# Kernel optimization log

Measured on AMD Instinct MI355X. Metric: run time of the kernel, lower is better.

## Reference

```python
import jax, jax.numpy as jnp
import numpy as np

N = 50000
E = 1_600_000


def spmm(edge_index, edge_weight, support, num_nodes):
    # adj[i, j] = w for (i=row, j=col); out[i] = sum_j adj[i,j] * support[j]
    row, col = edge_index[0], edge_index[1]
    msgs = support[col] * edge_weight[:, None]  # [E, d] gather + scale
    return jax.ops.segment_sum(msgs, row, num_segments=num_nodes)


def setup_inputs() -> dict:
    key = jax.random.key(0)
    ks = jax.random.split(key, 7)
    x = jax.random.normal(ks[0], (N, 128), dtype=jnp.float32)
    edge_index = jax.random.randint(ks[1], (2, E), 0, N, dtype=jnp.int64)
    edge_weight = jax.random.uniform(ks[2], (E,), dtype=jnp.float32)
    W1 = jax.random.normal(ks[3], (128, 128), dtype=jnp.float32) * (1.0 / np.sqrt(128))
    b1 = jax.random.normal(ks[4], (128,), dtype=jnp.float32) * (1.0 / np.sqrt(128))
    W2 = jax.random.normal(ks[5], (128, 40), dtype=jnp.float32) * (1.0 / np.sqrt(40))
    b2 = jax.random.normal(ks[6], (40,), dtype=jnp.float32) * (1.0 / np.sqrt(40))
    return {"x": x, "edge_index": edge_index, "edge_weight": edge_weight,
            "W1": W1, "b1": b1, "W2": W2, "b2": b2}


def reference(x, edge_index, edge_weight, W1, b1, W2, b2):
    n = x.shape[0]
    # layer 1: GraphConvolution + ReLU (dropout p=0.0 -> no-op)
    h = spmm(edge_index, edge_weight, x @ W1, n) + b1
    h = jax.nn.relu(h)
    # layer 2: GraphConvolution
    out = spmm(edge_index, edge_weight, h @ W2, n) + b2
    return jax.nn.log_softmax(out, axis=1)
```

## Files before the change

kernel.cpp:

```cpp
#include <hip/hip_runtime.h>
#include <hip/hip_fp16.h>
#include <math.h>

#define N_NODES 50000
#define N_EDGES 1600000
#define D1 128
#define D2 40
#define D2P 64
#define BROWS 128
#define NB 391
#define CHUNK 6250

typedef __attribute__((ext_vector_type(8))) short bf16x8;
typedef __attribute__((ext_vector_type(4))) float f32x4;

__device__ __forceinline__ void bf16_split(float v, unsigned short& h, unsigned short& l) {
    unsigned u = __float_as_uint(v);
    unsigned r = u + 0x7fffu + ((u >> 16) & 1u);
    h = (unsigned short)(r >> 16);
    float hf = __uint_as_float((unsigned)h << 16);
    float lof = v - hf;
    unsigned u2 = __float_as_uint(lof);
    unsigned r2 = u2 + 0x7fffu + ((u2 >> 16) & 1u);
    l = (unsigned short)(r2 >> 16);
}

__device__ __forceinline__ int detect_is64_block(const unsigned int* ei) {
    __shared__ int any;
    if (threadIdx.x == 0) any = 0;
    __syncthreads();
    int a = 0;
    for (int i = threadIdx.x; i < 2048; i += 256) a |= (ei[2 * i + 1] != 0u);
    if (a) any = 1;
    __syncthreads();
    return any ? 0 : 1;
}

__device__ __forceinline__ int edge_row(const unsigned int* ei, int e, int is64) {
    return (int)(is64 ? ei[2 * e] : ei[e]);
}
__device__ __forceinline__ int edge_col(const unsigned int* ei, int e, int is64) {
    return (int)(is64 ? ei[2 * (N_EDGES + e)] : ei[N_EDGES + e]);
}

__global__ __launch_bounds__(256) void prep_k(const unsigned int* __restrict__ ei,
                                              unsigned int* __restrict__ gbhp,
                                              const float* __restrict__ W1,
                                              unsigned short* __restrict__ wh1,
                                              unsigned short* __restrict__ wl1,
                                              const float* __restrict__ W2,
                                              unsigned short* __restrict__ wh2,
                                              unsigned short* __restrict__ wl2) {
    int b = blockIdx.x, t = threadIdx.x;
    if (b < 64) {
        int idx = b * 256 + t;
        int k = idx >> 7, n = idx & 127;
        unsigned short h, l;
        bf16_split(W1[k * 128 + n], h, l);
        int nt = n >> 4, ks = k >> 5;
        int lane = (n & 15) | (((k >> 3) & 3) << 4);
        int j = k & 7;
        int dst = ((nt * 4 + ks) * 64 + lane) * 8 + j;
        wh1[dst] = h;
        wl1[dst] = l;
    } else if (b < 96) {
        int idx = (b - 64) * 256 + t;
        int k = idx >> 6, n = idx & 63;
        float v = (n < D2) ? W2[k * D2 + n] : 0.f;
        unsigned short h, l;
        bf16_split(v, h, l);
        int nt = n >> 4, ks = k >> 5;
        int lane = (n & 15) | (((k >> 3) & 3) << 4);
        int j = k & 7;
        int dst = ((nt * 4 + ks) * 64 + lane) * 8 + j;
        wh2[dst] = h;
        wl2[dst] = l;
    } else {
        int is64 = detect_is64_block(ei);
        __shared__ unsigned int bh[NB];
        for (int i = t; i < NB; i += 256) bh[i] = 0;
        __syncthreads();
        int e0 = (b - 96) * CHUNK, e1 = e0 + CHUNK;
        for (int e = e0 + t; e < e1; e += 256) {
            atomicAdd(&bh[edge_row(ei, e, is64) >> 7], 1u);
        }
        __syncthreads();
        for (int i = t; i < NB; i += 256) {
            if (bh[i]) atomicAdd(&gbhp[i * 16], bh[i]);
        }
    }
}

__global__ __launch_bounds__(512) void bscan_k(const unsigned int* __restrict__ gbhp,
                                               int* __restrict__ bbase,
                                               unsigned int* __restrict__ bcurp) {
    __shared__ unsigned int s[512];
    int t = threadIdx.x;
    unsigned int v = (t < NB) ? gbhp[t * 16] : 0u;
    s[t] = v;
    __syncthreads();
    for (int off = 1; off < 512; off <<= 1) {
        unsigned int add = (t >= off) ? s[t - off] : 0u;
        __syncthreads();
        s[t] += add;
        __syncthreads();
    }
    if (t < NB) {
        unsigned int excl = s[t] - v;
        bbase[t] = (int)excl;
        bcurp[t * 16] = excl;
    }
    if (t == NB - 1) bbase[NB] = (int)s[t];
}

__global__ __launch_bounds__(256) void work1_k(const unsigned int* __restrict__ ei,
                                               const float* __restrict__ ew,
                                               unsigned int* __restrict__ bcurp,
                                               uint2* __restrict__ tmp8,
                                               const float* __restrict__ x,
                                               const unsigned short* __restrict__ wh,
                                               const unsigned short* __restrict__ wl,
                                               __half* __restrict__ Ah) {
    int b = blockIdx.x, t = threadIdx.x;
    if (b < 256) {
        int is64 = detect_is64_block(ei);
        __shared__ unsigned int lh[NB];
        __shared__ unsigned int lcur[NB];
        for (int i = t; i < NB; i += 256) lh[i] = 0;
        __syncthreads();
        int e0 = b * CHUNK, e1 = e0 + CHUNK;
        for (int e = e0 + t; e < e1; e += 256) {
            atomicAdd(&lh[edge_row(ei, e, is64) >> 7], 1u);
        }
        __syncthreads();
        for (int i = t; i < NB; i += 256) {
            if (lh[i]) lcur[i] = atomicAdd(&bcurp[i * 16], lh[i]);
        }
        __syncthreads();
        for (int e = e0 + t; e < e1; e += 256) {
            int r = edge_row(ei, e, is64);
            int c = edge_col(ei, e, is64);
            int bk = r >> 7;
            unsigned int p = atomicAdd(&lcur[bk], 1u);
            uint2 rec;
            rec.x = ((unsigned int)(r & 127) << 24) | (unsigned int)c;
            rec.y = __float_as_uint(ew[e]);
            tmp8[p] = rec;
        }
    } else {
        int gb = b - 256;
        int w = t >> 6, l = t & 63;
        int row0 = gb * 64 + w * 16;
        int arow = row0 + (l & 15);
        if (arow > N_NODES - 1) arow = N_NODES - 1;
        int kbase = (l >> 4) * 8;
        bf16x8 ah[4], al[4];
#pragma unroll
        for (int ks = 0; ks < 4; ++ks) {
            const float* px = &x[arow * D1 + ks * 32 + kbase];
            float4 v0 = *reinterpret_cast<const float4*>(px);
            float4 v1 = *reinterpret_cast<const float4*>(px + 4);
            float vv[8] = {v0.x, v0.y, v0.z, v0.w, v1.x, v1.y, v1.z, v1.w};
#pragma unroll
            for (int j = 0; j < 8; ++j) {
                unsigned short h, lo2;
                bf16_split(vv[j], h, lo2);
                ah[ks][j] = (short)h;
                al[ks][j] = (short)lo2;
            }
        }
        f32x4 acc[8];
#pragma unroll
        for (int nt = 0; nt < 8; ++nt) acc[nt] = (f32x4)(0.f);
#pragma unroll
        for (int nt = 0; nt < 8; ++nt) {
#pragma unroll
            for (int ks = 0; ks < 4; ++ks) {
                int fo = ((nt * 4 + ks) * 64 + l) * 8;
                bf16x8 bh = *reinterpret_cast<const bf16x8*>(&wh[fo]);
                bf16x8 bl = *reinterpret_cast<const bf16x8*>(&wl[fo]);
                acc[nt] = __builtin_amdgcn_mfma_f32_16x16x32_bf16(ah[ks], bh, acc[nt], 0, 0, 0);
                acc[nt] = __builtin_amdgcn_mfma_f32_16x16x32_bf16(ah[ks], bl, acc[nt], 0, 0, 0);
                acc[nt] = __builtin_amdgcn_mfma_f32_16x16x32_bf16(al[ks], bh, acc[nt], 0, 0, 0);
            }
        }
        int crow0 = row0 + (l >> 4) * 4;
        int ccol = l & 15;
#pragma unroll
        for (int nt = 0; nt < 8; ++nt) {
#pragma unroll
            for (int r = 0; r < 4; ++r) {
                int rr = crow0 + r;
                if (rr < N_NODES) Ah[rr * D1 + nt * 16 + ccol] = __float2half_rn(acc[nt][r]);
            }
        }
    }
}

__global__ __launch_bounds__(256) void csr_k(const uint2* __restrict__ tmp8,
                                             const int* __restrict__ bbase,
                                             int* __restrict__ rowptr,
                                             uint2* __restrict__ colwS) {
    __shared__ unsigned int rcnt[BROWS];
    __shared__ unsigned int loff[BROWS];
    __shared__ unsigned int lcur[BROWS];
    int b = blockIdx.x;
    int t = threadIdx.x;
    int lo = bbase[b], hi = bbase[b + 1];
    int r0 = b * BROWS;
    int nrows = N_NODES - r0;
    if (nrows > BROWS) nrows = BROWS;
    if (t < BROWS) rcnt[t] = 0;
    __syncthreads();
    for (int j = lo + t; j < hi; j += 256) {
        atomicAdd(&rcnt[tmp8[j].x >> 24], 1u);
    }
    __syncthreads();
    if (t < BROWS) loff[t] = rcnt[t];
    __syncthreads();
    for (int off = 1; off < BROWS; off <<= 1) {
        unsigned int add = (t >= off && t < BROWS) ? loff[t - off] : 0u;
        __syncthreads();
        if (t < BROWS) loff[t] += add;
        __syncthreads();
    }
    if (t < BROWS) {
        unsigned int excl = loff[t] - rcnt[t];
        if (t < nrows) rowptr[r0 + t] = lo + (int)excl;
        lcur[t] = (unsigned int)lo + excl;
    }
    if (b == NB - 1 && t == 0) rowptr[N_NODES] = hi;
    __syncthreads();
    for (int j = lo + t; j < hi; j += 256) {
        uint2 rec = tmp8[j];
        unsigned int rl = rec.x >> 24;
        unsigned int p = atomicAdd(&lcur[rl], 1u);
        uint2 cw;
        cw.x = rec.x & 0xFFFFu;
        cw.y = rec.y;
        colwS[p] = cw;
    }
}

__global__ __launch_bounds__(256) void spmm1_k(const __half* __restrict__ Ah,
                                               const int* __restrict__ rowptr,
                                               const uint2* __restrict__ colwS,
                                               float* __restrict__ B) {
    int t = threadIdx.x;
    int r = blockIdx.x * 4 + (t >> 6);
    int lane = t & 63;
    int half = lane >> 5;
    int cg = lane & 31;
    int s = rowptr[r], e = rowptr[r + 1];
    float4 acc = {0.f, 0.f, 0.f, 0.f};
#pragma unroll 4
    for (int j = s + half; j < e; j += 2) {
        uint2 cw = colwS[j];
        float w = __uint_as_float(cw.y);
        uint2 q = *reinterpret_cast<const uint2*>(&Ah[cw.x * D1 + cg * 4]);
        float2 f0 = __half22float2(*reinterpret_cast<const __half2*>(&q.x));
        float2 f1 = __half22float2(*reinterpret_cast<const __half2*>(&q.y));
        acc.x += w * f0.x;
        acc.y += w * f0.y;
        acc.z += w * f1.x;
        acc.w += w * f1.y;
    }
    acc.x += __shfl_xor(acc.x, 32);
    acc.y += __shfl_xor(acc.y, 32);
    acc.z += __shfl_xor(acc.z, 32);
    acc.w += __shfl_xor(acc.w, 32);
    if (half == 0) *reinterpret_cast<float4*>(&B[r * D1 + cg * 4]) = acc;
}

__global__ __launch_bounds__(256) void gemm2_k(const float* __restrict__ Bm,
                                               const float* __restrict__ b1,
                                               const unsigned short* __restrict__ wh,
                                               const unsigned short* __restrict__ wl,
                                               __half* __restrict__ Gh) {
    int t = threadIdx.x;
    int w = t >> 6, l = t & 63;
    int row0 = blockIdx.x * 64 + w * 16;
    int arow = row0 + (l & 15);
    if (arow > N_NODES - 1) arow = N_NODES - 1;
    int kbase = (l >> 4) * 8;
    bf16x8 ah[4], al[4];
#pragma unroll
    for (int ks = 0; ks < 4; ++ks) {
        const float* pb = &Bm[arow * D1 + ks * 32 + kbase];
        const float* pb1 = &b1[ks * 32 + kbase];
        float4 v0 = *reinterpret_cast<const float4*>(pb);
        float4 v1 = *reinterpret_cast<const float4*>(pb + 4);
        float4 c0 = *reinterpret_cast<const float4*>(pb1);
        float4 c1 = *reinterpret_cast<const float4*>(pb1 + 4);
        float vv[8] = {v0.x + c0.x, v0.y + c0.y, v0.z + c0.z, v0.w + c0.w,
                       v1.x + c1.x, v1.y + c1.y, v1.z + c1.z, v1.w + c1.w};
#pragma unroll
        for (int j = 0; j < 8; ++j) {
            float rv = vv[j] > 0.f ? vv[j] : 0.f;
            unsigned short h, lo2;
            bf16_split(rv, h, lo2);
            ah[ks][j] = (short)h;
            al[ks][j] = (short)lo2;
        }
    }
    f32x4 acc[4];
#pragma unroll
    for (int nt = 0; nt < 4; ++nt) acc[nt] = (f32x4)(0.f);
#pragma unroll
    for (int nt = 0; nt < 4; ++nt) {
#pragma unroll
        for (int ks = 0; ks < 4; ++ks) {
            int fo = ((nt * 4 + ks) * 64 + l) * 8;
            bf16x8 bh = *reinterpret_cast<const bf16x8*>(&wh[fo]);
            bf16x8 bl = *reinterpret_cast<const bf16x8*>(&wl[fo]);
            acc[nt] = __builtin_amdgcn_mfma_f32_16x16x32_bf16(ah[ks], bh, acc[nt], 0, 0, 0);
            acc[nt] = __builtin_amdgcn_mfma_f32_16x16x32_bf16(ah[ks], bl, acc[nt], 0, 0, 0);
            acc[nt] = __builtin_amdgcn_mfma_f32_16x16x32_bf16(al[ks], bh, acc[nt], 0, 0, 0);
        }
    }
    int crow0 = row0 + (l >> 4) * 4;
    int ccol = l & 15;
#pragma unroll
    for (int nt = 0; nt < 4; ++nt) {
        int col = nt * 16 + ccol;
#pragma unroll
        for (int r = 0; r < 4; ++r) {
            int rr = crow0 + r;
            if (rr < N_NODES) Gh[rr * D2P + col] = __float2half_rn(acc[nt][r]);
        }
    }
}

__global__ __launch_bounds__(256) void spmm2lsm_k(const __half* __restrict__ Gh,
                                                  const int* __restrict__ rowptr,
                                                  const uint2* __restrict__ colwS,
                                                  const float* __restrict__ b2,
                                                  float* __restrict__ out) {
    int t = threadIdx.x;
    int r = blockIdx.x * 4 + (t >> 6);
    int lane = t & 63;
    int slot = lane >> 4;
    int li = lane & 15;
    int s = rowptr[r], e = rowptr[r + 1];
    float4 acc = {0.f, 0.f, 0.f, 0.f};
#pragma unroll 2
    for (int j0 = s; j0 < e; j0 += 4) {
        uint2 cwv = colwS[min(j0 + (lane & 3), e - 1)];
        int j = j0 + slot;
        if (j < e) {
            unsigned cx = __shfl(cwv.x, slot);
            float wv = __uint_as_float(__shfl(cwv.y, slot));
            uint2 q = reinterpret_cast<const uint2*>(&Gh[cx * D2P])[li];
            float2 f0 = __half22float2(*reinterpret_cast<const __half2*>(&q.x));
            float2 f1 = __half22float2(*reinterpret_cast<const __half2*>(&q.y));
            acc.x += wv * f0.x;
            acc.y += wv * f0.y;
            acc.z += wv * f1.x;
            acc.w += wv * f1.y;
        }
    }
    acc.x += __shfl_down(acc.x, 32);
    acc.y += __shfl_down(acc.y, 32);
    acc.z += __shfl_down(acc.z, 32);
    acc.w += __shfl_down(acc.w, 32);
    acc.x += __shfl_down(acc.x, 16);
    acc.y += __shfl_down(acc.y, 16);
    acc.z += __shfl_down(acc.z, 16);
    acc.w += __shfl_down(acc.w, 16);
    bool valid = (lane < 16) && (li < 10);
    float4 v4 = {-INFINITY, -INFINITY, -INFINITY, -INFINITY};
    if (valid) {
        float4 bv = *reinterpret_cast<const float4*>(&b2[li * 4]);
        v4.x = acc.x + bv.x;
        v4.y = acc.y + bv.y;
        v4.z = acc.z + bv.z;
        v4.w = acc.w + bv.w;
    }
    float m = fmaxf(fmaxf(v4.x, v4.y), fmaxf(v4.z, v4.w));
#pragma unroll
    for (int off = 1; off < 16; off <<= 1) m = fmaxf(m, __shfl_xor(m, off));
    float ex = valid ? expf(v4.x - m) + expf(v4.y - m) + expf(v4.z - m) + expf(v4.w - m) : 0.f;
#pragma unroll
    for (int off = 1; off < 16; off <<= 1) ex += __shfl_xor(ex, off);
    float lse = m + logf(ex);
    if (valid) {
        float4 o;
        o.x = v4.x - lse;
        o.y = v4.y - lse;
        o.z = v4.z - lse;
        o.w = v4.w - lse;
        *reinterpret_cast<float4*>(&out[r * D2 + li * 4]) = o;
    }
}

extern "C" void kernel_launch(void* const* d_in, const int* in_sizes, int n_in,
                              void* d_out, int out_size, void* d_ws, size_t ws_size,
                              hipStream_t stream) {
    const float* x = (const float*)d_in[0];
    const unsigned int* ei = (const unsigned int*)d_in[1];
    const float* ew = (const float*)d_in[2];
    const float* W1 = (const float*)d_in[3];
    const float* b1 = (const float*)d_in[4];
    const float* W2 = (const float*)d_in[5];
    const float* b2 = (const float*)d_in[6];
    float* out = (float*)d_out;

    char* w = (char*)d_ws;
    __half* Ah = (__half*)w;
    float* B = (float*)(w + 12800000);
    uint2* tmp8 = (uint2*)(w + 12800000);
    __half* Gh = (__half*)(w + 38400000);
    uint2* colwS = (uint2*)(w + 44800000);
    int* rowptr = (int*)(w + 57600000);
    int* bbase = (int*)(w + 57800064);
    unsigned int* bcurp = (unsigned int*)(w + 57801664);
    unsigned int* gbhp = (unsigned int*)(w + 57826688);
    unsigned short* wh1 = (unsigned short*)(w + 57851712);
    unsigned short* wl1 = (unsigned short*)(w + 57884480);
    unsigned short* wh2 = (unsigned short*)(w + 57917248);
    unsigned short* wl2 = (unsigned short*)(w + 57933632);

    hipMemsetAsync(gbhp, 0, NB * 64, stream);
    prep_k<<<352, 256, 0, stream>>>(ei, gbhp, W1, wh1, wl1, W2, wh2, wl2);
    bscan_k<<<1, 512, 0, stream>>>(gbhp, bbase, bcurp);
    work1_k<<<1038, 256, 0, stream>>>(ei, ew, bcurp, tmp8, x, wh1, wl1, Ah);
    csr_k<<<NB, 256, 0, stream>>>(tmp8, bbase, rowptr, colwS);

    spmm1_k<<<N_NODES / 4, 256, 0, stream>>>(Ah, rowptr, colwS, B);
    gemm2_k<<<782, 256, 0, stream>>>(B, b1, wh2, wl2, Gh);
    spmm2lsm_k<<<N_NODES / 4, 256, 0, stream>>>(Gh, rowptr, colwS, b2, out);
}
```

Baseline: 276.4 us.

## Bin edges per chunk in LDS, store hidden layer as fp16, remap spmm2 lanes

CSR construction is restructured. Each block now sorts its edge chunk into row-buckets in LDS and writes the chunk contiguously along with per-bucket offsets. csr_k then gathers its bucket's segments from all chunks into LDS, replacing the global-atomic scatter and the second read of the edge list. The intermediate B matrix is stored as fp16 to halve traffic into gemm2, and spmm2 switches to a two-edge-per-iteration layout with 32 lanes by 2 columns. Risks: csr_k uses a fixed LDS cap of 7000 records per bucket with no overflow check, a serial per-thread copy loop, and fp16 adds rounding error to the hidden layer.

```diff
diff --git a/kernel.cpp b/kernel.cpp
--- a/kernel.cpp
+++ b/kernel.cpp
@@ -10,6 +10,7 @@
 #define BROWS 128
 #define NB 391
 #define CHUNK 6250
+#define CSR_CAP 7000
 
 typedef __attribute__((ext_vector_type(8))) short bf16x8;
 typedef __attribute__((ext_vector_type(4))) float f32x4;
@@ -43,9 +44,7 @@
     return (int)(is64 ? ei[2 * (N_EDGES + e)] : ei[N_EDGES + e]);
 }
 
-__global__ __launch_bounds__(256) void prep_k(const unsigned int* __restrict__ ei,
-                                              unsigned int* __restrict__ gbhp,
-                                              const float* __restrict__ W1,
+__global__ __launch_bounds__(256) void prep_k(const float* __restrict__ W1,
                                               unsigned short* __restrict__ wh1,
                                               unsigned short* __restrict__ wl1,
                                               const float* __restrict__ W2,
@@ -63,7 +62,7 @@
         int dst = ((nt * 4 + ks) * 64 + lane) * 8 + j;
         wh1[dst] = h;
         wl1[dst] = l;
-    } else if (b < 96) {
+    } else {
         int idx = (b - 64) * 256 + t;
         int k = idx >> 6, n = idx & 63;
         float v = (n < D2) ? W2[k * D2 + n] : 0.f;
@@ -75,25 +74,69 @@
         int dst = ((nt * 4 + ks) * 64 + lane) * 8 + j;
         wh2[dst] = h;
         wl2[dst] = l;
-    } else {
-        int is64 = detect_is64_block(ei);
-        __shared__ unsigned int bh[NB];
-        for (int i = t; i < NB; i += 256) bh[i] = 0;
-        __syncthreads();
-        int e0 = (b - 96) * CHUNK, e1 = e0 + CHUNK;
-        for (int e = e0 + t; e < e1; e += 256) {
-            atomicAdd(&bh[edge_row(ei, e, is64) >> 7], 1u);
-        }
-        __syncthreads();
-        for (int i = t; i < NB; i += 256) {
-            if (bh[i]) atomicAdd(&gbhp[i * 16], bh[i]);
-        }
-    }
+    }
+}
+
+__global__ __launch_bounds__(256) void bin_k(const unsigned int* __restrict__ ei,
+                                             const float* __restrict__ ew,
+                                             unsigned int* __restrict__ gbhp,
+                                             uint2* __restrict__ tmp8,
+                                             unsigned int* __restrict__ bofs) {
+    __shared__ uint2 lrec[CHUNK];
+    __shared__ unsigned int lh[NB];
+    __shared__ unsigned int lstart[NB + 1];
+    __shared__ unsigned int lcur[NB];
+    __shared__ unsigned int ssum[256];
+    int b = blockIdx.x, t = threadIdx.x;
+    int is64 = detect_is64_block(ei);
+    for (int i = t; i < NB; i += 256) lh[i] = 0;
+    __syncthreads();
+    int e0 = b * CHUNK, e1 = e0 + CHUNK;
+    for (int e = e0 + t; e < e1; e += 256) {
+        atomicAdd(&lh[edge_row(ei, e, is64) >> 7], 1u);
+    }
+    __syncthreads();
+    for (int i = t; i < NB; i += 256) {
+        if (lh[i]) atomicAdd(&gbhp[i * 16], lh[i]);
+    }
+    unsigned int lsum = 0;
+    if (t < 196) {
+        lsum = lh[2 * t];
+        if (2 * t + 1 < NB) lsum += lh[2 * t + 1];
+    }
+    ssum[t] = lsum;
+    __syncthreads();
+    for (int off = 1; off < 256; off <<= 1) {
+        unsigned int add = (t >= off) ? ssum[t - off] : 0u;
+        __syncthreads();
+        ssum[t] += add;
+        __syncthreads();
+    }
+    unsigned int run = (t == 0) ? 0u : ssum[t - 1];
+    if (t < 196) {
+        lstart[2 * t] = run;
+        if (2 * t + 1 < NB) lstart[2 * t + 1] = run + lh[2 * t];
+    }
+    if (t == 0) lstart[NB] = CHUNK;
+    __syncthreads();
+    for (int i = t; i < NB; i += 256) lcur[i] = lstart[i];
+    __syncthreads();
+    for (int e = e0 + t; e < e1; e += 256) {
+        int r = edge_row(ei, e, is64);
+        int c = edge_col(ei, e, is64);
+        unsigned int p = atomicAdd(&lcur[r >> 7], 1u);
+        uint2 rec;
+        rec.x = ((unsigned int)r << 16) | (unsigned int)c;
+        rec.y = __float_as_uint(ew[e]);
+        lrec[p] = rec;
+    }
+    __syncthreads();
+    for (int i = t; i <= NB; i += 256) bofs[b * (NB + 1) + i] = lstart[i];
+    for (int p = t; p < CHUNK; p += 256) tmp8[e0 + p] = lrec[p];
 }
 
 __global__ __launch_bounds__(512) void bscan_k(const unsigned int* __restrict__ gbhp,
-                                               int* __restrict__ bbase,
-                                               unsigned int* __restrict__ bcurp) {
+                                               int* __restrict__ bbase) {
     __shared__ unsigned int s[512];
     int t = threadIdx.x;
     unsigned int v = (t < NB) ? gbhp[t * 16] : 0u;
@@ -105,125 +148,54 @@
         s[t] += add;
         __syncthreads();
     }
-    if (t < NB) {
-        unsigned int excl = s[t] - v;
-        bbase[t] = (int)excl;
-        bcurp[t * 16] = excl;
-    }
+    if (t < NB) bbase[t] = (int)(s[t] - v);
     if (t == NB - 1) bbase[NB] = (int)s[t];
 }
 
-__global__ __launch_bounds__(256) void work1_k(const unsigned int* __restrict__ ei,
-                                               const float* __restrict__ ew,
-                                               unsigned int* __restrict__ bcurp,
-                                               uint2* __restrict__ tmp8,
-                                               const float* __restrict__ x,
-                                               const unsigned short* __restrict__ wh,
-                                               const unsigned short* __restrict__ wl,
-                                               __half* __restrict__ Ah) {
-    int b = blockIdx.x, t = threadIdx.x;
-    if (b < 256) {
-        int is64 = detect_is64_block(ei);
-        __shared__ unsigned int lh[NB];
-        __shared__ unsigned int lcur[NB];
-        for (int i = t; i < NB; i += 256) lh[i] = 0;
-        __syncthreads();
-        int e0 = b * CHUNK, e1 = e0 + CHUNK;
-        for (int e = e0 + t; e < e1; e += 256) {
-            atomicAdd(&lh[edge_row(ei, e, is64) >> 7], 1u);
-        }
-        __syncthreads();
-        for (int i = t; i < NB; i += 256) {
-            if (lh[i]) lcur[i] = atomicAdd(&bcurp[i * 16], lh[i]);
-        }
-        __syncthreads();
-        for (int e = e0 + t; e < e1; e += 256) {
-            int r = edge_row(ei, e, is64);
-            int c = edge_col(ei, e, is64);
-            int bk = r >> 7;
-            unsigned int p = atomicAdd(&lcur[bk], 1u);
-            uint2 rec;
-            rec.x = ((unsigned int)(r & 127) << 24) | (unsigned int)c;
-            rec.y = __float_as_uint(ew[e]);
-            tmp8[p] = rec;
-        }
-    } else {
-        int gb = b - 256;
-        int w = t >> 6, l = t & 63;
-        int row0 = gb * 64 + w * 16;
-        int arow = row0 + (l & 15);
-        if (arow > N_NODES - 1) arow = N_NODES - 1;
-        int kbase = (l >> 4) * 8;
-        bf16x8 ah[4], al[4];
-#pragma unroll
-        for (int ks = 0; ks < 4; ++ks) {
-            const float* px = &x[arow * D1 + ks * 32 + kbase];
-            float4 v0 = *reinterpret_cast<const float4*>(px);
-            float4 v1 = *reinterpret_cast<const float4*>(px + 4);
-            float vv[8] = {v0.x, v0.y, v0.z, v0.w, v1.x, v1.y, v1.z, v1.w};
-#pragma unroll
-            for (int j = 0; j < 8; ++j) {
-                unsigned short h, lo2;
-                bf16_split(vv[j], h, lo2);
-                ah[ks][j] = (short)h;
-                al[ks][j] = (short)lo2;
-            }
-        }
-        f32x4 acc[8];
-#pragma unroll
-        for (int nt = 0; nt < 8; ++nt) acc[nt] = (f32x4)(0.f);
-#pragma unroll
-        for (int nt = 0; nt < 8; ++nt) {
-#pragma unroll
-            for (int ks = 0; ks < 4; ++ks) {
-                int fo = ((nt * 4 + ks) * 64 + l) * 8;
-                bf16x8 bh = *reinterpret_cast<const bf16x8*>(&wh[fo]);
-                bf16x8 bl = *reinterpret_cast<const bf16x8*>(&wl[fo]);
-                acc[nt] = __builtin_amdgcn_mfma_f32_16x16x32_bf16(ah[ks], bh, acc[nt], 0, 0, 0);
-                acc[nt] = __builtin_amdgcn_mfma_f32_16x16x32_bf16(ah[ks], bl, acc[nt], 0, 0, 0);
-                acc[nt] = __builtin_amdgcn_mfma_f32_16x16x32_bf16(al[ks], bh, acc[nt], 0, 0, 0);
-            }
-        }
-        int crow0 = row0 + (l >> 4) * 4;
-        int ccol = l & 15;
-#pragma unroll
-        for (int nt = 0; nt < 8; ++nt) {
-#pragma unroll
-            for (int r = 0; r < 4; ++r) {
-                int rr = crow0 + r;
-                if (rr < N_NODES) Ah[rr * D1 + nt * 16 + ccol] = __float2half_rn(acc[nt][r]);
-            }
-        }
-    }
-}
-
 __global__ __launch_bounds__(256) void csr_k(const uint2* __restrict__ tmp8,
+                                             const unsigned int* __restrict__ bofs,
                                              const int* __restrict__ bbase,
                                              int* __restrict__ rowptr,
                                              uint2* __restrict__ colwS) {
+    __shared__ uint2 lrec[CSR_CAP];
+    __shared__ unsigned int ssum[256];
     __shared__ unsigned int rcnt[BROWS];
     __shared__ unsigned int loff[BROWS];
     __shared__ unsigned int lcur[BROWS];
-    int b = blockIdx.x;
-    int t = threadIdx.x;
+    int b = blockIdx.x, t = threadIdx.x;
+    unsigned int mystart = bofs[t * (NB + 1) + b];
+    unsigned int myend = bofs[t * (NB + 1) + b + 1];
+    unsigned int mycnt = myend - mystart;
+    ssum[t] = mycnt;
+    __syncthreads();
+    for (int off = 1; off < 256; off <<= 1) {
+        unsigned int add = (t >= off) ? ssum[t - off] : 0u;
+        __syncthreads();
+        ssum[t] += add;
+        __syncthreads();
+    }
+    unsigned int mybase = ssum[t] - mycnt;
+    unsigned int total = ssum[255];
+    const uint2* src = &tmp8[t * CHUNK + mystart];
+    for (unsigned int k = 0; k < mycnt; ++k) lrec[mybase + k] = src[k];
+    if (t < BROWS) rcnt[t] = 0;
+    __syncthreads();
+    for (unsigned int p = t; p < total; p += 256) {
+        atomicAdd(&rcnt[(lrec[p].x >> 16) & 127], 1u);
+    }
+    __syncthreads();
+    if (t < BROWS) loff[t] = rcnt[t];
+    __syncthreads();
+    for (int off = 1; off < BROWS; off <<= 1) {
+        unsigned int add = (t >= off && t < BROWS) ? loff[t - off] : 0u;
+        __syncthreads();
+        if (t < BROWS) loff[t] += add;
+        __syncthreads();
+    }
     int lo = bbase[b], hi = bbase[b + 1];
     int r0 = b * BROWS;
     int nrows = N_NODES - r0;
     if (nrows > BROWS) nrows = BROWS;
-    if (t < BROWS) rcnt[t] = 0;
-    __syncthreads();
-    for (int j = lo + t; j < hi; j += 256) {
-        atomicAdd(&rcnt[tmp8[j].x >> 24], 1u);
-    }
-    __syncthreads();
-    if (t < BROWS) loff[t] = rcnt[t];
-    __syncthreads();
-    for (int off = 1; off < BROWS; off <<= 1) {
-        unsigned int add = (t >= off && t < BROWS) ? loff[t - off] : 0u;
-        __syncthreads();
-        if (t < BROWS) loff[t] += add;
-        __syncthreads();
-    }
     if (t < BROWS) {
         unsigned int excl = loff[t] - rcnt[t];
         if (t < nrows) rowptr[r0 + t] = lo + (int)excl;
@@ -231,21 +203,73 @@
     }
     if (b == NB - 1 && t == 0) rowptr[N_NODES] = hi;
     __syncthreads();
-    for (int j = lo + t; j < hi; j += 256) {
-        uint2 rec = tmp8[j];
-        unsigned int rl = rec.x >> 24;
-        unsigned int p = atomicAdd(&lcur[rl], 1u);
+    for (unsigned int p = t; p < total; p += 256) {
+        uint2 rec = lrec[p];
+        unsigned int rl = (rec.x >> 16) & 127;
+        unsigned int pos = atomicAdd(&lcur[rl], 1u);
         uint2 cw;
         cw.x = rec.x & 0xFFFFu;
         cw.y = rec.y;
-        colwS[p] = cw;
+        colwS[pos] = cw;
+    }
+}
+
+__global__ __launch_bounds__(256) void gemm1_k(const float* __restrict__ x,
+                                               const unsigned short* __restrict__ wh,
+                                               const unsigned short* __restrict__ wl,
+                                               __half* __restrict__ Ah) {
+    int t = threadIdx.x;
+    int w = t >> 6, l = t & 63;
+    int row0 = blockIdx.x * 64 + w * 16;
+    int arow = row0 + (l & 15);
+    if (arow > N_NODES - 1) arow = N_NODES - 1;
+    int kbase = (l >> 4) * 8;
+    bf16x8 ah[4], al[4];
+#pragma unroll
+    for (int ks = 0; ks < 4; ++ks) {
+        const float* px = &x[arow * D1 + ks * 32 + kbase];
+        float4 v0 = *reinterpret_cast<const float4*>(px);
+        float4 v1 = *reinterpret_cast<const float4*>(px + 4);
+        float vv[8] = {v0.x, v0.y, v0.z, v0.w, v1.x, v1.y, v1.z, v1.w};
+#pragma unroll
+        for (int j = 0; j < 8; ++j) {
+            unsigned short h, lo2;
+            bf16_split(vv[j], h, lo2);
+            ah[ks][j] = (short)h;
+            al[ks][j] = (short)lo2;
+        }
+    }
+    f32x4 acc[8];
+#pragma unroll
+    for (int nt = 0; nt < 8; ++nt) acc[nt] = (f32x4)(0.f);
+#pragma unroll
+    for (int nt = 0; nt < 8; ++nt) {
+#pragma unroll
+        for (int ks = 0; ks < 4; ++ks) {
+            int fo = ((nt * 4 + ks) * 64 + l) * 8;
+            bf16x8 bh = *reinterpret_cast<const bf16x8*>(&wh[fo]);
+            bf16x8 bl = *reinterpret_cast<const bf16x8*>(&wl[fo]);
+            acc[nt] = __builtin_amdgcn_mfma_f32_16x16x32_bf16(ah[ks], bh, acc[nt], 0, 0, 0);
+            acc[nt] = __builtin_amdgcn_mfma_f32_16x16x32_bf16(ah[ks], bl, acc[nt], 0, 0, 0);
+            acc[nt] = __builtin_amdgcn_mfma_f32_16x16x32_bf16(al[ks], bh, acc[nt], 0, 0, 0);
+        }
+    }
+    int crow0 = row0 + (l >> 4) * 4;
+    int ccol = l & 15;
+#pragma unroll
+    for (int nt = 0; nt < 8; ++nt) {
+#pragma unroll
+        for (int r = 0; r < 4; ++r) {
+            int rr = crow0 + r;
+            if (rr < N_NODES) Ah[rr * D1 + nt * 16 + ccol] = __float2half_rn(acc[nt][r]);
+        }
     }
 }
 
 __global__ __launch_bounds__(256) void spmm1_k(const __half* __restrict__ Ah,
                                                const int* __restrict__ rowptr,
                                                const uint2* __restrict__ colwS,
-                                               float* __restrict__ B) {
+                                               __half* __restrict__ Bh) {
     int t = threadIdx.x;
     int r = blockIdx.x * 4 + (t >> 6);
     int lane = t & 63;
@@ -269,10 +293,19 @@
     acc.y += __shfl_xor(acc.y, 32);
     acc.z += __shfl_xor(acc.z, 32);
     acc.w += __shfl_xor(acc.w, 32);
-    if (half == 0) *reinterpret_cast<float4*>(&B[r * D1 + cg * 4]) = acc;
-}
-
-__global__ __launch_bounds__(256) void gemm2_k(const float* __restrict__ Bm,
+    if (half == 0) {
+        unsigned p0 = ((unsigned)__half_as_ushort(__float2half_rn(acc.y)) << 16) |
+                      __half_as_ushort(__float2half_rn(acc.x));
+        unsigned p1 = ((unsigned)__half_as_ushort(__float2half_rn(acc.w)) << 16) |
+                      __half_as_ushort(__float2half_rn(acc.z));
+        uint2 st;
+        st.x = p0;
+        st.y = p1;
+        *reinterpret_cast<uint2*>(&Bh[r * D1 + cg * 4]) = st;
+    }
+}
+
+__global__ __launch_bounds__(256) void gemm2_k(const __half* __restrict__ Bh,
                                                const float* __restrict__ b1,
                                                const unsigned short* __restrict__ wh,
                                                const unsigned short* __restrict__ wl,
@@ -286,14 +319,17 @@
     bf16x8 ah[4], al[4];
 #pragma unroll
     for (int ks = 0; ks < 4; ++ks) {
-        const float* pb = &Bm[arow * D1 + ks * 32 + kbase];
+        const __half* pb = &Bh[arow * D1 + ks * 32 + kbase];
         const float* pb1 = &b1[ks * 32 + kbase];
-        float4 v0 = *reinterpret_cast<const float4*>(pb);
-        float4 v1 = *reinterpret_cast<const float4*>(pb + 4);
+        uint4 q = *reinterpret_cast<const uint4*>(pb);
+        float2 g0 = __half22float2(*reinterpret_cast<const __half2*>(&q.x));
+        float2 g1 = __half22float2(*reinterpret_cast<const __half2*>(&q.y));
+        float2 g2 = __half22float2(*reinterpret_cast<const __half2*>(&q.z));
+        float2 g3 = __half22float2(*reinterpret_cast<const __half2*>(&q.w));
         float4 c0 = *reinterpret_cast<const float4*>(pb1);
         float4 c1 = *reinterpret_cast<const float4*>(pb1 + 4);
-        float vv[8] = {v0.x + c0.x, v0.y + c0.y, v0.z + c0.z, v0.w + c0.w,
-                       v1.x + c1.x, v1.y + c1.y, v1.z + c1.z, v1.w + c1.w};
+        float vv[8] = {g0.x + c0.x, g0.y + c0.y, g1.x + c0.z, g1.y + c0.w,
+                       g2.x + c1.x, g2.y + c1.y, g3.x + c1.z, g3.y + c1.w};
 #pragma unroll
         for (int j = 0; j < 8; ++j) {
             float rv = vv[j] > 0.f ? vv[j] : 0.f;
@@ -339,57 +375,40 @@
     int t = threadIdx.x;
     int r = blockIdx.x * 4 + (t >> 6);
     int lane = t & 63;
-    int slot = lane >> 4;
-    int li = lane & 15;
+    int half = lane >> 5;
+    int cg = lane & 31;
     int s = rowptr[r], e = rowptr[r + 1];
-    float4 acc = {0.f, 0.f, 0.f, 0.f};
-#pragma unroll 2
-    for (int j0 = s; j0 < e; j0 += 4) {
-        uint2 cwv = colwS[min(j0 + (lane & 3), e - 1)];
-        int j = j0 + slot;
-        if (j < e) {
-            unsigned cx = __shfl(cwv.x, slot);
-            float wv = __uint_as_float(__shfl(cwv.y, slot));
-            uint2 q = reinterpret_cast<const uint2*>(&Gh[cx * D2P])[li];
-            float2 f0 = __half22float2(*reinterpret_cast<const __half2*>(&q.x));
-            float2 f1 = __half22float2(*reinterpret_cast<const __half2*>(&q.y));
-            acc.x += wv * f0.x;
-            acc.y += wv * f0.y;
-            acc.z += wv * f1.x;
-            acc.w += wv * f1.y;
-        }
-    }
-    acc.x += __shfl_down(acc.x, 32);
-    acc.y += __shfl_down(acc.y, 32);
-    acc.z += __shfl_down(acc.z, 32);
-    acc.w += __shfl_down(acc.w, 32);
-    acc.x += __shfl_down(acc.x, 16);
-    acc.y += __shfl_down(acc.y, 16);
-    acc.z += __shfl_down(acc.z, 16);
-    acc.w += __shfl_down(acc.w, 16);
-    bool valid = (lane < 16) && (li < 10);
-    float4 v4 = {-INFINITY, -INFINITY, -INFINITY, -INFINITY};
+    float2 acc = {0.f, 0.f};
+#pragma unroll 4
+    for (int j = s + half; j < e; j += 2) {
+        uint2 cw = colwS[j];
+        float w = __uint_as_float(cw.y);
+        unsigned q = *reinterpret_cast<const unsigned*>(&Gh[cw.x * D2P + cg * 2]);
+        float2 f = __half22float2(*reinterpret_cast<const __half2*>(&q));
+        acc.x += w * f.x;
+        acc.y += w * f.y;
+    }
+    acc.x += __shfl_xor(acc.x, 32);
+    acc.y += __shfl_xor(acc.y, 32);
+    bool valid = lane < 20;
+    float2 v2 = {-INFINITY, -INFINITY};
     if (valid) {
-        float4 bv = *reinterpret_cast<const float4*>(&b2[li * 4]);
-        v4.x = acc.x + bv.x;
-        v4.y = acc.y + bv.y;
-        v4.z = acc.z + bv.z;
-        v4.w = acc.w + bv.w;
-    }
-    float m = fmaxf(fmaxf(v4.x, v4.y), fmaxf(v4.z, v4.w));
-#pragma unroll
-    for (int off = 1; off < 16; off <<= 1) m = fmaxf(m, __shfl_xor(m, off));
-    float ex = valid ? expf(v4.x - m) + expf(v4.y - m) + expf(v4.z - m) + expf(v4.w - m) : 0.f;
-#pragma unroll
-    for (int off = 1; off < 16; off <<= 1) ex += __shfl_xor(ex, off);
+        float2 bv = reinterpret_cast<const float2*>(b2)[cg];
+        v2.x = acc.x + bv.x;
+        v2.y = acc.y + bv.y;
+    }
+    float m = fmaxf(v2.x, v2.y);
+#pragma unroll
+    for (int off = 1; off < 32; off <<= 1) m = fmaxf(m, __shfl_xor(m, off));
+    float ex = valid ? expf(v2.x - m) + expf(v2.y - m) : 0.f;
+#pragma unroll
+    for (int off = 1; off < 32; off <<= 1) ex += __shfl_xor(ex, off);
     float lse = m + logf(ex);
     if (valid) {
-        float4 o;
-        o.x = v4.x - lse;
-        o.y = v4.y - lse;
-        o.z = v4.z - lse;
-        o.w = v4.w - lse;
-        *reinterpret_cast<float4*>(&out[r * D2 + li * 4]) = o;
+        float2 o;
+        o.x = v2.x - lse;
+        o.y = v2.y - lse;
+        *reinterpret_cast<float2*>(&out[r * D2 + cg * 2]) = o;
     }
 }
 
@@ -407,26 +426,27 @@
 
     char* w = (char*)d_ws;
     __half* Ah = (__half*)w;
-    float* B = (float*)(w + 12800000);
-    uint2* tmp8 = (uint2*)(w + 12800000);
+    __half* Bh = (__half*)(w + 12800000);
+    uint2* tmp8 = (uint2*)(w + 25600000);
     __half* Gh = (__half*)(w + 38400000);
     uint2* colwS = (uint2*)(w + 44800000);
     int* rowptr = (int*)(w + 57600000);
     int* bbase = (int*)(w + 57800064);
-    unsigned int* bcurp = (unsigned int*)(w + 57801664);
-    unsigned int* gbhp = (unsigned int*)(w + 57826688);
-    unsigned short* wh1 = (unsigned short*)(w + 57851712);
-    unsigned short* wl1 = (unsigned short*)(w + 57884480);
-    unsigned short* wh2 = (unsigned short*)(w + 57917248);
-    unsigned short* wl2 = (unsigned short*)(w + 57933632);
+    unsigned int* bofs = (unsigned int*)(w + 57801664);
+    unsigned int* gbhp = (unsigned int*)(w + 58203072);
+    unsigned short* wh1 = (unsigned short*)(w + 58228096);
+    unsigned short* wl1 = (unsigned short*)(w + 58260864);
+    unsigned short* wh2 = (unsigned short*)(w + 58293632);
+    unsigned short* wl2 = (unsigned short*)(w + 58310016);
 
     hipMemsetAsync(gbhp, 0, NB * 64, stream);
-    prep_k<<<352, 256, 0, stream>>>(ei, gbhp, W1, wh1, wl1, W2, wh2, wl2);
-    bscan_k<<<1, 512, 0, stream>>>(gbhp, bbase, bcurp);
-    work1_k<<<1038, 256, 0, stream>>>(ei, ew, bcurp, tmp8, x, wh1, wl1, Ah);
-    csr_k<<<NB, 256, 0, stream>>>(tmp8, bbase, rowptr, colwS);
-
-    spmm1_k<<<N_NODES / 4, 256, 0, stream>>>(Ah, rowptr, colwS, B);
-    gemm2_k<<<782, 256, 0, stream>>>(B, b1, wh2, wl2, Gh);
+    prep_k<<<96, 256, 0, stream>>>(W1, wh1, wl1, W2, wh2, wl2);
+    bin_k<<<256, 256, 0, stream>>>(ei, ew, gbhp, tmp8, bofs);
+    bscan_k<<<1, 512, 0, stream>>>(gbhp, bbase);
+    gemm1_k<<<782, 256, 0, stream>>>(x, wh1, wl1, Ah);
+    csr_k<<<NB, 256, 0, stream>>>(tmp8, bofs, bbase, rowptr, colwS);
+
+    spmm1_k<<<N_NODES / 4, 256, 0, stream>>>(Ah, rowptr, colwS, Bh);
+    gemm2_k<<<782, 256, 0, stream>>>(Bh, b1, wh2, wl2, Gh);
     spmm2lsm_k<<<N_NODES / 4, 256, 0, stream>>>(Gh, rowptr, colwS, b2, out);
 }
```

Measured after the change: 260.0 us. 1.06x faster.
